# Kernel tuning notes

Hardware: AMD Instinct MI355X
Metric: run time of the kernel (lower is better)

## Reference

```python
import jax, jax.numpy as jnp
import numpy as np

SR = 16000
NUM_MEL = 80
FRAME_LEN = 400
FRAME_SHIFT = 160
PADDED_WIN = 512         # next pow2 of 400
NUM_FFT_BINS = PADDED_WIN // 2 + 1  # 257
PREEMPH = 0.97
EPS = 1e-6


def _mel_scale(f):
    return 1127.0 * np.log(1.0 + f / 700.0)


def _get_mel_banks(num_bins, window_padded, sample_freq, low_freq=20.0, high_freq=0.0):
    # Faithful port of torchaudio.compliance.kaldi.get_mel_banks (vtln_warp=1.0)
    num_fft_bins = window_padded // 2  # 256 (last bin padded with zero later)
    nyquist = 0.5 * sample_freq
    if high_freq <= 0.0:
        high_freq = nyquist + high_freq
    fft_bin_width = sample_freq / window_padded
    mel_low = _mel_scale(low_freq)
    mel_high = _mel_scale(high_freq)
    mel_delta = (mel_high - mel_low) / (num_bins + 1)
    left = mel_low + np.arange(num_bins, dtype=np.float64)[:, None] * mel_delta
    center = left + mel_delta
    right = center + mel_delta
    mel = _mel_scale(fft_bin_width * np.arange(num_fft_bins, dtype=np.float64))[None, :]
    up = (mel - left) / (center - left)
    down = (right - mel) / (right - center)
    bins = np.maximum(0.0, np.minimum(up, down))
    return bins.astype(np.float32)  # [num_bins, window_padded//2]


def _make_buffers():
    n = np.arange(FRAME_LEN, dtype=np.float32)
    window = (0.54 - 0.46 * np.cos(2 * np.pi * n / (FRAME_LEN - 1))).astype(np.float32)
    t = np.arange(PADDED_WIN, dtype=np.float32)
    f = np.arange(NUM_FFT_BINS, dtype=np.float32)[:, None]
    angles = 2.0 * np.pi * f * t / PADDED_WIN
    dft_real = np.cos(angles).astype(np.float32)        # [257, 512]
    dft_imag = (-np.sin(angles)).astype(np.float32)     # [257, 512]
    mel = _get_mel_banks(NUM_MEL, PADDED_WIN, float(SR))
    mel_weight = np.pad(mel, ((0, 0), (0, 1)))          # [80, 257]
    return window, dft_real, dft_imag, mel_weight


def setup_inputs() -> dict:
    key = jax.random.key(0)
    waveform = jax.random.normal(key, (32, 480000), dtype=jnp.float32)
    window, dft_real, dft_imag, mel_weight = _make_buffers()
    return {
        "waveform": waveform,
        "window": jnp.asarray(window),
        "dft_real": jnp.asarray(dft_real),
        "dft_imag": jnp.asarray(dft_imag),
        "mel_weight": jnp.asarray(mel_weight),
    }


def reference(waveform, window, dft_real, dft_imag, mel_weight):
    B, T = waveform.shape
    num_frames = (T - FRAME_LEN) // FRAME_SHIFT + 1
    # Framing (equivalent to conv1d with identity kernel, stride=FRAME_SHIFT)
    idx = jnp.arange(num_frames)[:, None] * FRAME_SHIFT + jnp.arange(FRAME_LEN)
    frames = waveform[:, idx].reshape(B * num_frames, FRAME_LEN)  # [BF, 400]
    # dither == 0 -> skipped
    # remove DC offset
    frames = frames - jnp.mean(frames, axis=1, keepdims=True)
    # raw energy (computed by the original module; unused since use_energy=False)
    _log_energy = jnp.log(jnp.maximum(jnp.sum(frames * frames, axis=1), EPS))
    # preemphasis with replicate left pad
    prev = jnp.concatenate([frames[:, :1], frames[:, :-1]], axis=1)
    frames = frames - PREEMPH * prev
    # Hamming window + zero pad to 512
    frames = frames * window[None, :]
    frames = jnp.pad(frames, ((0, 0), (0, PADDED_WIN - FRAME_LEN)))  # [BF, 512]
    # Brute-force DFT as matmuls
    real = frames @ dft_real.T  # [BF, 257]
    imag = frames @ dft_imag.T  # [BF, 257]
    power = real * real + imag * imag
    # Mel projection + log
    mel = power @ mel_weight.T + EPS  # [BF, 80]
    mel = jnp.log(jnp.maximum(mel, EPS))
    return mel.reshape(B, num_frames, NUM_MEL)
```

## Files before the change

### kernel.cpp

```cpp
#include <hip/hip_runtime.h>
#include <math.h>


#define BATCH 32
#define TLEN 480000
#define NFRAMES 2998
#define FL 400
#define FS 160
#define PW 512
#define NM 80
#define MT 32
#define NTILES 94
#define PRE 0.97f
#define EPSF 1e-6f

#define RE_KS 9
#define IM_KS 8
#define RE_U16 (16 * RE_KS * 64 * 8)
#define IM_U16 (16 * IM_KS * 64 * 8)
#define MEL_U16 (6 * 8 * 64 * 8)
#define OFF_REH 0
#define OFF_REL RE_U16
#define OFF_IMH (2 * RE_U16)
#define OFF_IML (2 * RE_U16 + IM_U16)
#define OFF_MEL (2 * RE_U16 + 2 * IM_U16)
#define OFF_CS  (OFF_MEL + MEL_U16)
#define WS_NEED ((size_t)OFF_CS * 2 + 512 * 4)

#define C0_SH 0
#define C0_SL 8704
#define C0_DH 17408
#define C0_DL 26112
#define C1_SH 0
#define C1_SL 10240
#define C1_DH 20480
#define C1_DL 29184

typedef short bf16x8 __attribute__((ext_vector_type(8)));
typedef float f32x4 __attribute__((ext_vector_type(4)));
typedef unsigned int u32;
typedef unsigned short u16;
typedef u32 u32x4 __attribute__((ext_vector_type(4)));

__device__ __forceinline__ u16 f2bf(float f) {
    u32 u = __builtin_bit_cast(u32, f);
    return (u16)((u + 0x7FFFu + ((u >> 16) & 1u)) >> 16);
}
__device__ __forceinline__ float bf2f(u16 h) {
    u32 u = ((u32)h) << 16;
    return __builtin_bit_cast(float, u);
}

__global__ void prep_kernel(const float* __restrict__ dftr, const float* __restrict__ dfti,
                            const float* __restrict__ melw, u16* __restrict__ wsb) {
    int idx = blockIdx.x * 256 + threadIdx.x;
    if (idx < 16 * RE_KS * 64) {
        int nf = idx / (RE_KS * 64);
        int rem = idx - nf * (RE_KS * 64);
        int ks = rem >> 6, l = rem & 63;
        int f = nf * 16 + (l & 15);
        int k = ks * 32 + ((l >> 4) << 3);
        u16* dh = wsb + OFF_REH + (size_t)idx * 8;
        u16* dl = wsb + OFF_REL + (size_t)idx * 8;
        #pragma unroll
        for (int e = 0; e < 8; ++e) {
            int kk = k + e;
            float x = (kk <= 256) ? dftr[(size_t)f * PW + kk] : 0.f;
            u16 h = f2bf(x);
            dh[e] = h;
            dl[e] = f2bf(x - bf2f(h));
        }
    } else if (idx < 16 * RE_KS * 64 + 16 * IM_KS * 64) {
        int j = idx - 16 * RE_KS * 64;
        int nf = j / (IM_KS * 64);
        int rem = j - nf * (IM_KS * 64);
        int ks = rem >> 6, l = rem & 63;
        int f = nf * 16 + (l & 15);
        int k = ks * 32 + ((l >> 4) << 3);
        u16* dh = wsb + OFF_IMH + (size_t)j * 8;
        u16* dl = wsb + OFF_IML + (size_t)j * 8;
        #pragma unroll
        for (int e = 0; e < 8; ++e) {
            float x = dfti[(size_t)f * PW + k + e];
            u16 h = f2bf(x);
            dh[e] = h;
            dl[e] = f2bf(x - bf2f(h));
        }
    } else {
        int m = idx - (16 * RE_KS * 64 + 16 * IM_KS * 64);
        if (m < 6 * 8 * 64) {
            int nf = m / (8 * 64);
            int ks = (m >> 6) & 7, l = m & 63;
            int n = nf * 16 + (l & 15);
            int k = ks * 32 + ((l >> 4) << 3);
            u16* dst = wsb + OFF_MEL + (size_t)m * 8;
            #pragma unroll
            for (int e = 0; e < 8; ++e)
                dst[e] = (n < NM) ? f2bf(melw[(size_t)n * 257 + k + e]) : (u16)0;
        }
    }
}

__global__ void prep_cs_kernel(const float* __restrict__ dftr, const float* __restrict__ dfti,
                               const float* __restrict__ win, u16* __restrict__ wsb) {
    const int gw = (blockIdx.x * 256 + threadIdx.x) >> 6;
    const int lane = threadIdx.x & 63;
    float* cs = (float*)(wsb + OFF_CS);
    float acc = 0.f;
    if (gw < 256) {
        const int f = gw;
        for (int t = lane; t <= 256; t += 64) {
            float wt = (t < FL) ? win[t] : 0.f;
            float wu = (t >= 1 && t < 256 && (512 - t) < FL) ? win[512 - t] : 0.f;
            acc += (wt + wu) * dftr[(size_t)f * PW + t];
        }
    } else {
        const int ff = gw - 256;
        for (int t = lane; t <= 255; t += 64) {
            float wt = (t < FL) ? win[t] : 0.f;
            float wu = (t >= 1 && (512 - t) < FL) ? win[512 - t] : 0.f;
            acc += (wt - wu) * dfti[(size_t)ff * PW + t];
        }
    }
    #pragma unroll
    for (int o = 32; o; o >>= 1) acc += __shfl_xor(acc, o);
    if (lane == 0) cs[gw] = acc;
}

__device__ __forceinline__ u32 swz(int SWT, u32 r) {
    return (SWT == 0) ? ((r & 7u) << 4) : (SWT == 1) ? (((r >> 1) & 3u) << 4) : 0u;
}

#define MFMA6(D, J)                                                                        \
    _Pragma("unroll")                                                                      \
    for (int mf = 0; mf < 2; ++mf) {                                                       \
        acc[mf][J] = __builtin_amdgcn_mfma_f32_16x16x32_bf16(aH[mf], D[0], acc[mf][J], 0, 0, 0); \
        acc[mf][J] = __builtin_amdgcn_mfma_f32_16x16x32_bf16(aL[mf], D[0], acc[mf][J], 0, 0, 0); \
        acc[mf][J] = __builtin_amdgcn_mfma_f32_16x16x32_bf16(aH[mf], D[1], acc[mf][J], 0, 0, 0); \
    }

template<int RS, int SWT, int NKS, int BKS>
__device__ __forceinline__ void dft_pass(
    const char* tH, const char* tL,
    const u16* __restrict__ bH, const u16* __restrict__ bL,
    int ks0, int g, int lane, f32x4 (&acc)[2][4]) {

    bf16x8 aH[2], aL[2], Ba[2], Bb[2];

#define LDA_P(KS)                                                              \
    { _Pragma("unroll")                                                        \
      for (int mf = 0; mf < 2; ++mf) {                                         \
        u32 r = (u32)(mf * 16 + (lane & 15));                                  \
        u32 off = (u32)((KS) * 64 + ((lane >> 4) << 4));                       \
        u32 byte = r * RS + (off ^ swz(SWT, r));                               \
        aH[mf] = *(const bf16x8*)(tH + byte);                                  \
        aL[mf] = *(const bf16x8*)(tL + byte);                                  \
      } }
#define LDB_P(KSG, J, D)                                                       \
    {                                                                          \
        size_t o = ((size_t)((4 * g + (J)) * BKS + (KSG)) * 64 + lane) * 8;    \
        D[0] = *(const bf16x8*)(bH + o);                                       \
        D[1] = *(const bf16x8*)(bL + o);                                       \
    }

    LDB_P(ks0, 0, Ba);
    #pragma unroll
    for (int ks = 0; ks < NKS; ++ks) {
        LDA_P(ks);
        LDB_P(ks0 + ks, 1, Bb);
        MFMA6(Ba, 0);
        LDB_P(ks0 + ks, 2, Ba);
        MFMA6(Bb, 1);
        LDB_P(ks0 + ks, 3, Bb);
        MFMA6(Ba, 2);
        if (ks + 1 < NKS) LDB_P(ks0 + ks + 1, 0, Ba);
        MFMA6(Bb, 3);
    }
#undef LDA_P
#undef LDB_P
}

__device__ __forceinline__ void pack_write(const float* ys, char* baseH, char* baseL, u32 byte) {
    u32x4 hv, lv;
    #pragma unroll
    for (int e = 0; e < 4; ++e) {
        u16 h0 = f2bf(ys[2 * e]), h1 = f2bf(ys[2 * e + 1]);
        hv[e] = (u32)h0 | ((u32)h1 << 16);
        u16 l0 = f2bf(ys[2 * e] - bf2f(h0)), l1 = f2bf(ys[2 * e + 1] - bf2f(h1));
        lv[e] = (u32)l0 | ((u32)l1 << 16);
    }
    *(u32x4*)(baseH + byte) = hv;
    *(u32x4*)(baseL + byte) = lv;
}

__global__ __launch_bounds__(256, 3) void fbank_mfma(
    const float* __restrict__ wave, const float* __restrict__ win,
    const u16* __restrict__ wsb, float* __restrict__ out) {
    __shared__ float smean[MT];
    __shared__ u16 stile[18944];
    char* T = (char*)stile;

    const int tid = threadIdx.x, w = tid >> 6, lane = tid & 63;
    const int q = lane >> 4;
    const int cg = lane & 15;
    const int b = blockIdx.y;
    const int f0 = blockIdx.x * MT;
    const float* wb = wave + (size_t)b * TLEN;
    const float4* win4 = (const float4*)win;

    float ps[2] = {0.f, 0.f};

    #pragma unroll
    for (int i = 0; i < 2; ++i) {
        const int rr = w * 8 + i * 4 + q;
        const int fr = f0 + rr;
        const bool valid = fr < NFRAMES;
        const float* x = wb + (size_t)fr * FS;
        const float4* x4 = (const float4*)x;

        float4 v0 = {0,0,0,0}, v1 = {0,0,0,0};
        if (valid) { v0 = x4[2 * cg]; v1 = x4[2 * cg + 1]; }
        ps[i] += v0.x + v0.y + v0.z + v0.w + v1.x + v1.y + v1.z + v1.w;
        float4 w0 = win4[2 * cg], w1 = win4[2 * cg + 1];
        float xpn = __shfl(v1.w, lane - 1);
        float xprev = (cg == 0) ? v0.x : xpn;
        float y[8];
        y[0] = (v0.x - PRE * xprev) * w0.x;
        y[1] = (v0.y - PRE * v0.x) * w0.y;
        y[2] = (v0.z - PRE * v0.y) * w0.z;
        y[3] = (v0.w - PRE * v0.z) * w0.w;
        y[4] = (v1.x - PRE * v0.w) * w1.x;
        y[5] = (v1.y - PRE * v1.x) * w1.y;
        y[6] = (v1.z - PRE * v1.y) * w1.z;
        y[7] = (v1.w - PRE * v1.z) * w1.w;

        float yr[8];
        #pragma unroll
        for (int e = 0; e < 8; ++e) yr[e] = 0.f;
        if (cg >= 14) {
            const int u0 = 512 - 8 * cg;
            float4 xr0 = {0,0,0,0}, xr1 = {0,0,0,0};
            float xu0 = 0.f;
            if (valid) {
                xr0 = x4[u0 / 4 - 2]; xr1 = x4[u0 / 4 - 1];
                if (u0 <= 399) xu0 = x[u0];
            }
            ps[i] += xr0.x + xr0.y + xr0.z + xr0.w + xr1.x + xr1.y + xr1.z + xr1.w;
            float4 wr0 = win4[u0 / 4 - 2], wr1 = win4[u0 / 4 - 1];
            float wu0 = (u0 <= 399) ? win[u0] : 0.f;
            yr[0] = (xu0   - PRE * xr1.w) * wu0;
            yr[1] = (xr1.w - PRE * xr1.z) * wr1.w;
            yr[2] = (xr1.z - PRE * xr1.y) * wr1.z;
            yr[3] = (xr1.y - PRE * xr1.x) * wr1.y;
            yr[4] = (xr1.x - PRE * xr0.w) * wr1.x;
            yr[5] = (xr0.w - PRE * xr0.z) * wr0.w;
            yr[6] = (xr0.z - PRE * xr0.y) * wr0.z;
            yr[7] = (xr0.y - PRE * xr0.x) * wr0.y;
        }
        float s8[8], d8[8];
        #pragma unroll
        for (int e = 0; e < 8; ++e) { s8[e] = y[e] + yr[e]; d8[e] = y[e] - yr[e]; }
        u32 byte = (u32)rr * 272u + (u32)cg * 16u;
        pack_write(s8, T + C0_SH, T + C0_SL, byte);
        pack_write(d8, T + C0_DH, T + C0_DL, byte);
    }
    __syncthreads();

    const int g = w;
    f32x4 accR[2][4], accI[2][4];
    #pragma unroll
    for (int mf = 0; mf < 2; ++mf)
        #pragma unroll
        for (int j = 0; j < 4; ++j) { accR[mf][j] = (f32x4)0.f; accI[mf][j] = (f32x4)0.f; }

    dft_pass<272, 2, 4, RE_KS>(T + C0_SH, T + C0_SL, wsb + OFF_REH, wsb + OFF_REL, 0, g, lane, accR);
    dft_pass<272, 2, 4, IM_KS>(T + C0_DH, T + C0_DL, wsb + OFF_IMH, wsb + OFF_IML, 0, g, lane, accI);
    __syncthreads();

    #pragma unroll
    for (int i = 0; i < 2; ++i) {
        const int rr = w * 8 + i * 4 + q;
        const int fr = f0 + rr;
        const bool valid = fr < NFRAMES;
        const float* x = wb + (size_t)fr * FS;
        const float4* x4 = (const float4*)x;

        float4 v0 = {0,0,0,0}, v1 = {0,0,0,0};
        if (valid) { v0 = x4[32 + 2 * cg]; v1 = x4[33 + 2 * cg]; }
        ps[i] += v0.x + v0.y + v0.z + v0.w + v1.x + v1.y + v1.z + v1.w;
        float4 w0 = win4[32 + 2 * cg], w1 = win4[33 + 2 * cg];
        float xpn = __shfl(v1.w, lane - 1);
        float xprev = (cg == 0) ? (valid ? x[127] : 0.f) : xpn;
        float y[8];
        y[0] = (v0.x - PRE * xprev) * w0.x;
        y[1] = (v0.y - PRE * v0.x) * w0.y;
        y[2] = (v0.z - PRE * v0.y) * w0.z;
        y[3] = (v0.w - PRE * v0.z) * w0.w;
        y[4] = (v1.x - PRE * v0.w) * w1.x;
        y[5] = (v1.y - PRE * v1.x) * w1.y;
        y[6] = (v1.z - PRE * v1.y) * w1.z;
        y[7] = (v1.w - PRE * v1.z) * w1.w;

        const int u0 = 384 - 8 * cg;
        float4 xr0 = {0,0,0,0}, xr1 = {0,0,0,0};
        float xu0 = 0.f;
        if (valid) { xr0 = x4[u0 / 4 - 2]; xr1 = x4[u0 / 4 - 1]; xu0 = x[u0]; }
        ps[i] += xr0.x + xr0.y + xr0.z + xr0.w + xr1.x + xr1.y + xr1.z + xr1.w;
        float4 wr0 = win4[u0 / 4 - 2], wr1 = win4[u0 / 4 - 1];
        float wu0 = win[u0];
        float yr[8];
        yr[0] = (xu0   - PRE * xr1.w) * wu0;
        yr[1] = (xr1.w - PRE * xr1.z) * wr1.w;
        yr[2] = (xr1.z - PRE * xr1.y) * wr1.z;
        yr[3] = (xr1.y - PRE * xr1.x) * wr1.y;
        yr[4] = (xr1.x - PRE * xr0.w) * wr1.x;
        yr[5] = (xr0.w - PRE * xr0.z) * wr0.w;
        yr[6] = (xr0.z - PRE * xr0.y) * wr0.z;
        yr[7] = (xr0.y - PRE * xr0.x) * wr0.y;

        float s8[8], d8[8];
        #pragma unroll
        for (int e = 0; e < 8; ++e) { s8[e] = y[e] + yr[e]; d8[e] = y[e] - yr[e]; }
        u32 byteS = (u32)rr * 320u + (((u32)cg * 16u) ^ ((((u32)rr >> 1) & 3u) << 4));
        u32 byteD = (u32)rr * 272u + (u32)cg * 16u;
        pack_write(s8, T + C1_SH, T + C1_SL, byteS);
        pack_write(d8, T + C1_DH, T + C1_DL, byteD);

        float acc = ps[i];
        #pragma unroll
        for (int o = 8; o; o >>= 1) acc += __shfl_xor(acc, o);
        if (cg == 0) smean[rr] = acc * (1.0f / FL);
    }
    {
        const int rr = tid & 31;
        const int grp = tid >> 5;
        if (grp < 4) {
            const int fr = f0 + rr;
            float y256 = 0.f;
            if (grp == 0 && fr < NFRAMES) {
                const float* x = wb + (size_t)fr * FS;
                y256 = (x[256] - PRE * x[255]) * win[256];
            }
            float s8[8] = {y256, 0.f, 0.f, 0.f, 0.f, 0.f, 0.f, 0.f};
            u32 byte = (u32)rr * 320u + ((((u32)(16 + grp)) * 16u) ^ ((((u32)rr >> 1) & 3u) << 4));
            pack_write(s8, T + C1_SH, T + C1_SL, byte);
        }
    }
    __syncthreads();

    dft_pass<320, 1, 5, RE_KS>(T + C1_SH, T + C1_SL, wsb + OFF_REH, wsb + OFF_REL, 4, g, lane, accR);
    dft_pass<272, 2, 4, IM_KS>(T + C1_DH, T + C1_DL, wsb + OFF_IMH, wsb + OFF_IML, 4, g, lane, accI);
    __syncthreads();

    {
        const float* cs = (const float*)(wsb + OFF_CS);
        #pragma unroll
        for (int mf = 0; mf < 2; ++mf)
            #pragma unroll
            for (int j = 0; j < 4; ++j) {
                const u32 bin = (u32)(64 * g + j * 16 + cg);
                const float Cb = cs[bin], Sb = cs[256 + bin];
                #pragma unroll
                for (int r = 0; r < 4; ++r) {
                    u32 row = (u32)(mf * 16 + (q << 2) + r);
                    const float mcr = (1.0f - PRE) * smean[row];
                    float pR = accR[mf][j][r] - mcr * Cb;
                    float pI = accI[mf][j][r] - mcr * Sb;
                    float pw = pR * pR + pI * pI;
                    u32 byte = (row * 512u + bin * 2u) ^ ((row & 7u) << 4);
                    *(u16*)(T + byte) = f2bf(pw);
                }
            }
    }
    __syncthreads();

    const u16* melb = wsb + OFF_MEL;
    {
        const int mfm = w >> 1;
        const int nf0 = (w & 1) ? 3 : 0;
        f32x4 accM[3];
        #pragma unroll
        for (int j = 0; j < 3; ++j) accM[j] = (f32x4)0.f;
        for (int ks = 0; ks < 8; ++ks) {
            u32 row = (u32)(mfm * 16 + cg);
            u32 byte = (row * 512u + (u32)(ks * 32 + (q << 3)) * 2u) ^ ((row & 7u) << 4);
            bf16x8 aP = *(const bf16x8*)(T + byte);
            #pragma unroll
            for (int j = 0; j < 3; ++j) {
                bf16x8 bM = *(const bf16x8*)(melb + ((size_t)((nf0 + j) * 8 + ks) * 64 + lane) * 8);
                accM[j] = __builtin_amdgcn_mfma_f32_16x16x32_bf16(aP, bM, accM[j], 0, 0, 0);
            }
        }
        #pragma unroll
        for (int j = 0; j < 3; ++j) {
            const int m = (nf0 + j) * 16 + cg;
            #pragma unroll
            for (int r = 0; r < 4; ++r) {
                const int rowl = mfm * 16 + (q << 2) + r;
                const int fr = f0 + rowl;
                if (fr < NFRAMES && m < NM) {
                    float v = fmaxf(accM[j][r] + EPSF, EPSF);
                    out[((size_t)b * NFRAMES + fr) * NM + m] = logf(v);
                }
            }
        }
    }
}

#define TFB 16
#define NB 256
__global__ __launch_bounds__(256, 3) void fbank_fallback(
    const float* __restrict__ wave, const float* __restrict__ win,
    const float* __restrict__ dftr, const float* __restrict__ dfti,
    const float* __restrict__ melw, float* __restrict__ out) {
    __shared__ float s_fr[TFB][PW];
    __shared__ float s_pw[TFB][NB + 1];
    const int tid = threadIdx.x, wv = tid >> 6, lane = tid & 63;
    const int fbase = blockIdx.x * TFB;
    #pragma unroll
    for (int j = 0; j < TFB / 4; ++j) {
        const int lf = wv * (TFB / 4) + j;
        const int gid = fbase + lf;
        const int bb = gid / NFRAMES;
        const int fr = gid - bb * NFRAMES;
        const float* x = wave + (size_t)bb * TLEN + (size_t)fr * FS;
        float s = 0.f;
        for (int i = lane; i < FL; i += 64) s += x[i];
        #pragma unroll
        for (int off = 32; off >= 1; off >>= 1) s += __shfl_xor(s, off);
        const float mean = s * (1.0f / FL);
        for (int i = lane; i < FL; i += 64) {
            const float xi = x[i];
            const float xm = (i == 0) ? xi : x[i - 1];
            s_fr[lf][i] = (xi - PRE * xm - (1.0f - PRE) * mean) * win[i];
        }
        for (int i = FL + lane; i < PW; i += 64) s_fr[lf][i] = 0.f;
    }
    __syncthreads();
    {
        const int bin = tid;
        const float4* dr4 = (const float4*)(dftr + (size_t)bin * PW);
        const float4* di4 = (const float4*)(dfti + (size_t)bin * PW);
        float accr[TFB], acci[TFB];
        #pragma unroll
        for (int f = 0; f < TFB; ++f) { accr[f] = 0.f; acci[f] = 0.f; }
        for (int k4 = 0; k4 < PW / 4; ++k4) {
            const float4 r = dr4[k4], im = di4[k4];
            #pragma unroll
            for (int f = 0; f < TFB; ++f) {
                const float4 fr = *(const float4*)&s_fr[f][k4 * 4];
                accr[f] += fr.x * r.x + fr.y * r.y + fr.z * r.z + fr.w * r.w;
                acci[f] += fr.x * im.x + fr.y * im.y + fr.z * im.z + fr.w * im.w;
            }
        }
        #pragma unroll
        for (int f = 0; f < TFB; ++f) s_pw[f][bin] = accr[f] * accr[f] + acci[f] * acci[f];
    }
    __syncthreads();
    for (int o = tid; o < TFB * NM; o += 256) {
        const int f = o / NM, m = o - f * NM;
        const float* wm = melw + (size_t)m * 257;
        float acc = 0.f;
        for (int k = 0; k < NB; ++k) acc += s_pw[f][k] * wm[k];
        out[(size_t)(fbase + f) * NM + m] = logf(fmaxf(acc + EPSF, EPSF));
    }
}

extern "C" void kernel_launch(void* const* d_in, const int* in_sizes, int n_in,
                              void* d_out, int out_size, void* d_ws, size_t ws_size,
                              hipStream_t stream) {
    const float* wave = (const float*)d_in[0];
    const float* win  = (const float*)d_in[1];
    const float* dftr = (const float*)d_in[2];
    const float* dfti = (const float*)d_in[3];
    const float* melw = (const float*)d_in[4];
    float* out = (float*)d_out;

    if (ws_size >= WS_NEED) {
        u16* wsb = (u16*)d_ws;
        const int prep_threads = 16 * RE_KS * 64 + 16 * IM_KS * 64 + 6 * 8 * 64;
        prep_kernel<<<(prep_threads + 255) / 256, 256, 0, stream>>>(dftr, dfti, melw, wsb);
        prep_cs_kernel<<<128, 256, 0, stream>>>(dftr, dfti, win, wsb);
        dim3 grid(NTILES, BATCH);
        fbank_mfma<<<grid, 256, 0, stream>>>(wave, win, wsb, out);
    } else {
        const int nblocks = (BATCH * NFRAMES) / TFB;
        fbank_fallback<<<nblocks, 256, 0, stream>>>(wave, win, dftr, dfti, melw, out);
    }
}
```

Measured before the change: 128.7 us.

## Double block to 512 threads, splitting DFT bin columns across eight waves

The fused fbank kernel now launches 512 threads per block (8 waves) instead of 256. Each wave owns 32 frequency bins instead of 64, and each thread frames one row instead of two. The mel projection is re-split across six waves. The aim is more waves in flight per block and fewer accumulator registers per thread, to hide latency. In exchange there are more barriers across a larger block, and each wave reloads the A tile for fewer MFMAs, which raises LDS read traffic per flop.

```diff
diff --git a/kernel.cpp b/kernel.cpp
--- a/kernel.cpp
+++ b/kernel.cpp
@@ -143,7 +143,7 @@
 __device__ __forceinline__ void dft_pass(
     const char* tH, const char* tL,
     const u16* __restrict__ bH, const u16* __restrict__ bL,
-    int ks0, int g, int lane, f32x4 (&acc)[2][4]) {
+    int ks0, int w, int lane, f32x4 (&acc)[2][2]) {
 
     bf16x8 aH[2], aL[2], Ba[2], Bb[2];
 
@@ -158,7 +158,7 @@
       } }
 #define LDB_P(KSG, J, D)                                                       \
     {                                                                          \
-        size_t o = ((size_t)((4 * g + (J)) * BKS + (KSG)) * 64 + lane) * 8;    \
+        size_t o = ((size_t)((2 * w + (J)) * BKS + (KSG)) * 64 + lane) * 8;    \
         D[0] = *(const bf16x8*)(bH + o);                                       \
         D[1] = *(const bf16x8*)(bL + o);                                       \
     }
@@ -169,12 +169,8 @@
         LDA_P(ks);
         LDB_P(ks0 + ks, 1, Bb);
         MFMA6(Ba, 0);
-        LDB_P(ks0 + ks, 2, Ba);
+        if (ks + 1 < NKS) LDB_P(ks0 + ks + 1, 0, Ba);
         MFMA6(Bb, 1);
-        LDB_P(ks0 + ks, 3, Bb);
-        MFMA6(Ba, 2);
-        if (ks + 1 < NKS) LDB_P(ks0 + ks + 1, 0, Ba);
-        MFMA6(Bb, 3);
     }
 #undef LDA_P
 #undef LDB_P
@@ -193,7 +189,7 @@
     *(u32x4*)(baseL + byte) = lv;
 }
 
-__global__ __launch_bounds__(256, 3) void fbank_mfma(
+__global__ __launch_bounds__(512, 4) void fbank_mfma(
     const float* __restrict__ wave, const float* __restrict__ win,
     const u16* __restrict__ wsb, float* __restrict__ out) {
     __shared__ float smean[MT];
@@ -208,19 +204,17 @@
     const float* wb = wave + (size_t)b * TLEN;
     const float4* win4 = (const float4*)win;
 
-    float ps[2] = {0.f, 0.f};
-
-    #pragma unroll
-    for (int i = 0; i < 2; ++i) {
-        const int rr = w * 8 + i * 4 + q;
-        const int fr = f0 + rr;
-        const bool valid = fr < NFRAMES;
-        const float* x = wb + (size_t)fr * FS;
-        const float4* x4 = (const float4*)x;
-
+    const int rr = w * 4 + q;
+    const int fr = f0 + rr;
+    const bool valid = fr < NFRAMES;
+    const float* x = wb + (size_t)fr * FS;
+    const float4* x4 = (const float4*)x;
+    float ps = 0.f;
+
+    {
         float4 v0 = {0,0,0,0}, v1 = {0,0,0,0};
         if (valid) { v0 = x4[2 * cg]; v1 = x4[2 * cg + 1]; }
-        ps[i] += v0.x + v0.y + v0.z + v0.w + v1.x + v1.y + v1.z + v1.w;
+        ps += v0.x + v0.y + v0.z + v0.w + v1.x + v1.y + v1.z + v1.w;
         float4 w0 = win4[2 * cg], w1 = win4[2 * cg + 1];
         float xpn = __shfl(v1.w, lane - 1);
         float xprev = (cg == 0) ? v0.x : xpn;
@@ -245,7 +239,7 @@
                 xr0 = x4[u0 / 4 - 2]; xr1 = x4[u0 / 4 - 1];
                 if (u0 <= 399) xu0 = x[u0];
             }
-            ps[i] += xr0.x + xr0.y + xr0.z + xr0.w + xr1.x + xr1.y + xr1.z + xr1.w;
+            ps += xr0.x + xr0.y + xr0.z + xr0.w + xr1.x + xr1.y + xr1.z + xr1.w;
             float4 wr0 = win4[u0 / 4 - 2], wr1 = win4[u0 / 4 - 1];
             float wu0 = (u0 <= 399) ? win[u0] : 0.f;
             yr[0] = (xu0   - PRE * xr1.w) * wu0;
@@ -266,28 +260,20 @@
     }
     __syncthreads();
 
-    const int g = w;
-    f32x4 accR[2][4], accI[2][4];
+    f32x4 accR[2][2], accI[2][2];
     #pragma unroll
     for (int mf = 0; mf < 2; ++mf)
         #pragma unroll
-        for (int j = 0; j < 4; ++j) { accR[mf][j] = (f32x4)0.f; accI[mf][j] = (f32x4)0.f; }
-
-    dft_pass<272, 2, 4, RE_KS>(T + C0_SH, T + C0_SL, wsb + OFF_REH, wsb + OFF_REL, 0, g, lane, accR);
-    dft_pass<272, 2, 4, IM_KS>(T + C0_DH, T + C0_DL, wsb + OFF_IMH, wsb + OFF_IML, 0, g, lane, accI);
-    __syncthreads();
-
-    #pragma unroll
-    for (int i = 0; i < 2; ++i) {
-        const int rr = w * 8 + i * 4 + q;
-        const int fr = f0 + rr;
-        const bool valid = fr < NFRAMES;
-        const float* x = wb + (size_t)fr * FS;
-        const float4* x4 = (const float4*)x;
-
+        for (int j = 0; j < 2; ++j) { accR[mf][j] = (f32x4)0.f; accI[mf][j] = (f32x4)0.f; }
+
+    dft_pass<272, 2, 4, RE_KS>(T + C0_SH, T + C0_SL, wsb + OFF_REH, wsb + OFF_REL, 0, w, lane, accR);
+    dft_pass<272, 2, 4, IM_KS>(T + C0_DH, T + C0_DL, wsb + OFF_IMH, wsb + OFF_IML, 0, w, lane, accI);
+    __syncthreads();
+
+    {
         float4 v0 = {0,0,0,0}, v1 = {0,0,0,0};
         if (valid) { v0 = x4[32 + 2 * cg]; v1 = x4[33 + 2 * cg]; }
-        ps[i] += v0.x + v0.y + v0.z + v0.w + v1.x + v1.y + v1.z + v1.w;
+        ps += v0.x + v0.y + v0.z + v0.w + v1.x + v1.y + v1.z + v1.w;
         float4 w0 = win4[32 + 2 * cg], w1 = win4[33 + 2 * cg];
         float xpn = __shfl(v1.w, lane - 1);
         float xprev = (cg == 0) ? (valid ? x[127] : 0.f) : xpn;
@@ -305,7 +291,7 @@
         float4 xr0 = {0,0,0,0}, xr1 = {0,0,0,0};
         float xu0 = 0.f;
         if (valid) { xr0 = x4[u0 / 4 - 2]; xr1 = x4[u0 / 4 - 1]; xu0 = x[u0]; }
-        ps[i] += xr0.x + xr0.y + xr0.z + xr0.w + xr1.x + xr1.y + xr1.z + xr1.w;
+        ps += xr0.x + xr0.y + xr0.z + xr0.w + xr1.x + xr1.y + xr1.z + xr1.w;
         float4 wr0 = win4[u0 / 4 - 2], wr1 = win4[u0 / 4 - 1];
         float wu0 = win[u0];
         float yr[8];
@@ -326,30 +312,30 @@
         pack_write(s8, T + C1_SH, T + C1_SL, byteS);
         pack_write(d8, T + C1_DH, T + C1_DL, byteD);
 
-        float acc = ps[i];
+        float acc = ps;
         #pragma unroll
         for (int o = 8; o; o >>= 1) acc += __shfl_xor(acc, o);
         if (cg == 0) smean[rr] = acc * (1.0f / FL);
     }
     {
-        const int rr = tid & 31;
+        const int trr = tid & 31;
         const int grp = tid >> 5;
         if (grp < 4) {
-            const int fr = f0 + rr;
+            const int tfr = f0 + trr;
             float y256 = 0.f;
-            if (grp == 0 && fr < NFRAMES) {
-                const float* x = wb + (size_t)fr * FS;
-                y256 = (x[256] - PRE * x[255]) * win[256];
+            if (grp == 0 && tfr < NFRAMES) {
+                const float* tx = wb + (size_t)tfr * FS;
+                y256 = (tx[256] - PRE * tx[255]) * win[256];
             }
             float s8[8] = {y256, 0.f, 0.f, 0.f, 0.f, 0.f, 0.f, 0.f};
-            u32 byte = (u32)rr * 320u + ((((u32)(16 + grp)) * 16u) ^ ((((u32)rr >> 1) & 3u) << 4));
+            u32 byte = (u32)trr * 320u + ((((u32)(16 + grp)) * 16u) ^ ((((u32)trr >> 1) & 3u) << 4));
             pack_write(s8, T + C1_SH, T + C1_SL, byte);
         }
     }
     __syncthreads();
 
-    dft_pass<320, 1, 5, RE_KS>(T + C1_SH, T + C1_SL, wsb + OFF_REH, wsb + OFF_REL, 4, g, lane, accR);
-    dft_pass<272, 2, 4, IM_KS>(T + C1_DH, T + C1_DL, wsb + OFF_IMH, wsb + OFF_IML, 4, g, lane, accI);
+    dft_pass<320, 1, 5, RE_KS>(T + C1_SH, T + C1_SL, wsb + OFF_REH, wsb + OFF_REL, 4, w, lane, accR);
+    dft_pass<272, 2, 4, IM_KS>(T + C1_DH, T + C1_DL, wsb + OFF_IMH, wsb + OFF_IML, 4, w, lane, accI);
     __syncthreads();
 
     {
@@ -357,8 +343,8 @@
         #pragma unroll
         for (int mf = 0; mf < 2; ++mf)
             #pragma unroll
-            for (int j = 0; j < 4; ++j) {
-                const u32 bin = (u32)(64 * g + j * 16 + cg);
+            for (int j = 0; j < 2; ++j) {
+                const u32 bin = (u32)(32 * w + j * 16 + cg);
                 const float Cb = cs[bin], Sb = cs[256 + bin];
                 #pragma unroll
                 for (int r = 0; r < 4; ++r) {
@@ -375,32 +361,32 @@
     __syncthreads();
 
     const u16* melb = wsb + OFF_MEL;
-    {
-        const int mfm = w >> 1;
-        const int nf0 = (w & 1) ? 3 : 0;
-        f32x4 accM[3];
-        #pragma unroll
-        for (int j = 0; j < 3; ++j) accM[j] = (f32x4)0.f;
+    if (w < 6) {
+        const int mfm = w & 1;
+        const int nf0 = (w >> 1) * 2;
+        f32x4 accM[2];
+        #pragma unroll
+        for (int j = 0; j < 2; ++j) accM[j] = (f32x4)0.f;
         for (int ks = 0; ks < 8; ++ks) {
             u32 row = (u32)(mfm * 16 + cg);
             u32 byte = (row * 512u + (u32)(ks * 32 + (q << 3)) * 2u) ^ ((row & 7u) << 4);
             bf16x8 aP = *(const bf16x8*)(T + byte);
             #pragma unroll
-            for (int j = 0; j < 3; ++j) {
+            for (int j = 0; j < 2; ++j) {
                 bf16x8 bM = *(const bf16x8*)(melb + ((size_t)((nf0 + j) * 8 + ks) * 64 + lane) * 8);
                 accM[j] = __builtin_amdgcn_mfma_f32_16x16x32_bf16(aP, bM, accM[j], 0, 0, 0);
             }
         }
         #pragma unroll
-        for (int j = 0; j < 3; ++j) {
+        for (int j = 0; j < 2; ++j) {
             const int m = (nf0 + j) * 16 + cg;
             #pragma unroll
             for (int r = 0; r < 4; ++r) {
                 const int rowl = mfm * 16 + (q << 2) + r;
-                const int fr = f0 + rowl;
-                if (fr < NFRAMES && m < NM) {
+                const int ofr = f0 + rowl;
+                if (ofr < NFRAMES && m < NM) {
                     float v = fmaxf(accM[j][r] + EPSF, EPSF);
-                    out[((size_t)b * NFRAMES + fr) * NM + m] = logf(v);
+                    out[((size_t)b * NFRAMES + ofr) * NM + m] = logf(v);
                 }
             }
         }
@@ -482,7 +468,7 @@
         prep_kernel<<<(prep_threads + 255) / 256, 256, 0, stream>>>(dftr, dfti, melw, wsb);
         prep_cs_kernel<<<128, 256, 0, stream>>>(dftr, dfti, win, wsb);
         dim3 grid(NTILES, BATCH);
-        fbank_mfma<<<grid, 256, 0, stream>>>(wave, win, wsb, out);
+        fbank_mfma<<<grid, 512, 0, stream>>>(wave, win, wsb, out);
     } else {
         const int nblocks = (BATCH * NFRAMES) / TFB;
         fbank_fallback<<<nblocks, 256, 0, stream>>>(wave, win, dftr, dfti, melw, out);
```

New measurement: 119.1 us. -7.5%, faster.
